# Kernel optimization log

Measured on AMD Instinct MI355X. Metric: run time of the kernel, lower is better.

## Reference

```python
import jax, jax.numpy as jnp
import numpy as np

PROCESSING_SPEED = 8.0  # init kwarg: softmax temperature
EPS = 1e-8              # torch F.cosine_similarity eps
BATCH, SIZE, DIM = 1024, 65536, 512


def setup_inputs() -> dict:
    key = jax.random.key(0)
    k1, k2 = jax.random.split(key)
    x = jax.random.normal(k1, (BATCH, DIM), dtype=jnp.float32)
    memory_bank = jax.random.normal(k2, (SIZE, DIM), dtype=jnp.float32)
    return {"x": x, "memory_bank": memory_bank}


def reference(x, memory_bank):
    # Cosine similarity between every query and every memory row, computed as
    # normalized dot products (math-equivalent to F.cosine_similarity with
    # denominator clamp max(||a||*||b||, eps), avoiding the (B,S,D) broadcast).
    x_norm = jnp.linalg.norm(x, axis=1, keepdims=True)            # (B, 1)
    m_norm = jnp.linalg.norm(memory_bank, axis=1, keepdims=True)  # (S, 1)
    dots = jnp.einsum('bd,sd->bs', x, memory_bank)                # (B, S)
    sims = dots / jnp.maximum(x_norm * m_norm.T, EPS)             # (B, S)
    attention = jax.nn.softmax(sims * PROCESSING_SPEED, axis=1)   # (B, S)
    return attention @ memory_bank                                # (B, D)
```

## Files before the change

### kernel.cpp

```cpp
#include <hip/hip_runtime.h>
#include <hip/hip_bf16.h>
#include <stdint.h>

#define B_N 1024
#define S_N 65536
#define D_N 512
#define SCALE 8.0f
#define KSPLIT 16
#define KCHUNK (S_N / KSPLIT)

typedef __attribute__((ext_vector_type(8))) short bf16x8;
typedef __attribute__((ext_vector_type(4))) float f32x4;

#define OFF_MBF   ((size_t)0)
#define OFF_MT    (OFF_MBF + (size_t)S_N * D_N * 2)
#define OFF_XBF   (OFF_MT  + (size_t)D_N * S_N * 2)
#define OFF_P     (OFF_XBF + (size_t)B_N * D_N * 2)
#define OFF_XNSQ  (OFF_P   + (size_t)B_N * S_N * 2)
#define OFF_MNSQ  (OFF_XNSQ + (size_t)B_N * 4)
#define OFF_LSUM  (OFF_MNSQ + (size_t)S_N * 4)
#define OFF_OPART (OFF_LSUM + (size_t)B_N * 4)

__device__ __forceinline__ unsigned short f2bf(float f) {
  unsigned u = __builtin_bit_cast(unsigned, f);
  u += 0x7fffu + ((u >> 16) & 1u);
  return (unsigned short)(u >> 16);
}

__device__ __forceinline__ void stage16(const unsigned short* g, unsigned short* l) {
  __builtin_amdgcn_global_load_lds(
      (const __attribute__((address_space(1))) void*)g,
      (__attribute__((address_space(3))) void*)l, 16, 0, 0);
}

__global__ void k_prep_x(const float* __restrict__ X, unsigned short* __restrict__ Xbf,
                         float* __restrict__ xnsq) {
  const int row = blockIdx.x;
  const int t = threadIdx.x;
  float4 v = ((const float4*)(X + (size_t)row * D_N))[t];
  float ss = v.x*v.x + v.y*v.y + v.z*v.z + v.w*v.w;
  ushort4 o; o.x = f2bf(v.x); o.y = f2bf(v.y); o.z = f2bf(v.z); o.w = f2bf(v.w);
  ((ushort4*)(Xbf + (size_t)row * D_N))[t] = o;
  #pragma unroll
  for (int m = 1; m < 64; m <<= 1) ss += __shfl_xor(ss, m);
  __shared__ float partial[2];
  if ((t & 63) == 0) partial[t >> 6] = ss;
  __syncthreads();
  if (t == 0) xnsq[row] = partial[0] + partial[1];
}

__global__ void k_prep_m(const float* __restrict__ M, unsigned short* __restrict__ Mbf,
                         unsigned short* __restrict__ Mt, float* __restrict__ mnsq) {
  __shared__ float ts[64 * 65];
  const int t = threadIdx.x;
  const int s0 = blockIdx.x * 64;
  const int r = t >> 2, cq = t & 3;
  const int c = t >> 2, sq = t & 3;
  float ss = 0.f;
  for (int ct = 0; ct < 8; ++ct) {
    float f[16];
    const float4* src = (const float4*)(M + (size_t)(s0 + r) * D_N + ct * 64 + cq * 16);
    #pragma unroll
    for (int k = 0; k < 4; ++k) {
      float4 v = src[k];
      f[4*k+0] = v.x; f[4*k+1] = v.y; f[4*k+2] = v.z; f[4*k+3] = v.w;
    }
    union { unsigned short u[16]; uint4 v4[2]; } pk;
    #pragma unroll
    for (int j = 0; j < 16; ++j) {
      ss += f[j] * f[j];
      pk.u[j] = f2bf(f[j]);
      ts[r * 65 + cq * 16 + j] = f[j];
    }
    uint4* dst = (uint4*)(Mbf + (size_t)(s0 + r) * D_N + ct * 64 + cq * 16);
    dst[0] = pk.v4[0]; dst[1] = pk.v4[1];
    __syncthreads();
    union { unsigned short u[16]; uint4 v4[2]; } pt;
    #pragma unroll
    for (int j = 0; j < 16; ++j) pt.u[j] = f2bf(ts[(sq * 16 + j) * 65 + c]);
    uint4* dt = (uint4*)(Mt + (size_t)(ct * 64 + c) * S_N + s0 + sq * 16);
    dt[0] = pt.v4[0]; dt[1] = pt.v4[1];
    __syncthreads();
  }
  ss += __shfl_xor(ss, 1);
  ss += __shfl_xor(ss, 2);
  if (cq == 0) mnsq[s0 + r] = ss;
}

__global__ __launch_bounds__(256, 2) void k_qk(
    const unsigned short* __restrict__ Xbf, const unsigned short* __restrict__ Mbf,
    const float* __restrict__ xnsq, const float* __restrict__ mnsq,
    unsigned short* __restrict__ P, float* __restrict__ lsum) {
  __shared__ unsigned short As[128 * 64];
  __shared__ unsigned short Bs[128 * 64];
  const int t = threadIdx.x;
  const int w = t >> 6, lane = t & 63, quad = lane >> 4, l15 = lane & 15;
  const int wr = w >> 1, wc = w & 1;
  const int x7 = l15 & 7;
  const int bm = blockIdx.x, bn = blockIdx.y;

  f32x4 acc[4][4];
  #pragma unroll
  for (int i = 0; i < 4; ++i)
    #pragma unroll
    for (int j = 0; j < 4; ++j) acc[i][j] = (f32x4){0.f, 0.f, 0.f, 0.f};

  const int srow = t >> 3;
  const int schunk = (t & 7) ^ (srow & 7);
  const unsigned short* gA = Xbf + (size_t)(bm * 128 + srow) * D_N + schunk * 8;
  const unsigned short* gB = Mbf + (size_t)(bn * 128 + srow) * D_N + schunk * 8;
  unsigned short* lA = As + w * 512;
  unsigned short* lB = Bs + w * 512;

  for (int k0 = 0; k0 < D_N; k0 += 64) {
    #pragma unroll
    for (int i = 0; i < 4; ++i) {
      stage16(gA + (size_t)(i * 32) * D_N + k0, lA + i * 2048);
      stage16(gB + (size_t)(i * 32) * D_N + k0, lB + i * 2048);
    }
    __syncthreads();
    #pragma unroll
    for (int kk = 0; kk < 64; kk += 32) {
      const int cq = (kk >> 3) + quad;
      bf16x8 af[4], bfr[4];
      #pragma unroll
      for (int i = 0; i < 4; ++i)
        af[i] = *(const bf16x8*)&As[(wr * 64 + i * 16 + l15) * 64 + (cq ^ x7) * 8];
      #pragma unroll
      for (int j = 0; j < 4; ++j)
        bfr[j] = *(const bf16x8*)&Bs[(wc * 64 + j * 16 + l15) * 64 + (cq ^ x7) * 8];
      #pragma unroll
      for (int i = 0; i < 4; ++i)
        #pragma unroll
        for (int j = 0; j < 4; ++j)
          acc[i][j] = __builtin_amdgcn_mfma_f32_16x16x32_bf16(af[i], bfr[j], acc[i][j], 0, 0, 0);
    }
    __syncthreads();
  }

  float mn_[4];
  #pragma unroll
  for (int j = 0; j < 4; ++j) mn_[j] = mnsq[bn * 128 + wc * 64 + j * 16 + l15];
  #pragma unroll
  for (int i = 0; i < 4; ++i) {
    float rowsum[4];
    #pragma unroll
    for (int r = 0; r < 4; ++r) {
      const int b = bm * 128 + wr * 64 + i * 16 + quad * 4 + r;
      const float xq = xnsq[b];
      float rs = 0.f;
      #pragma unroll
      for (int j = 0; j < 4; ++j) {
        float d2 = fmaxf(xq * mn_[j], 1e-16f);
        float p = __expf(SCALE * acc[i][j][r] * rsqrtf(d2));
        rs += p;
        const int s = bn * 128 + wc * 64 + j * 16 + l15;
        P[(size_t)b * S_N + s] = f2bf(p);
      }
      rowsum[r] = rs;
    }
    #pragma unroll
    for (int r = 0; r < 4; ++r) {
      float rs = rowsum[r];
      rs += __shfl_xor(rs, 1);
      rs += __shfl_xor(rs, 2);
      rs += __shfl_xor(rs, 4);
      rs += __shfl_xor(rs, 8);
      if (l15 == 0) {
        const int b = bm * 128 + wr * 64 + i * 16 + quad * 4 + r;
        unsafeAtomicAdd(&lsum[b], rs);
      }
    }
  }
}

__global__ __launch_bounds__(256, 2) void k_pv(
    const unsigned short* __restrict__ P, const unsigned short* __restrict__ Mt,
    float* __restrict__ Opart) {
  __shared__ unsigned short As[128 * 64];
  __shared__ unsigned short Bs[128 * 64];
  const int t = threadIdx.x;
  const int w = t >> 6, lane = t & 63, quad = lane >> 4, l15 = lane & 15;
  const int wr = w >> 1, wc = w & 1;
  const int x7 = l15 & 7;
  const int bn = blockIdx.x, bm = blockIdx.y, ks = blockIdx.z;

  f32x4 acc[4][4];
  #pragma unroll
  for (int i = 0; i < 4; ++i)
    #pragma unroll
    for (int j = 0; j < 4; ++j) acc[i][j] = (f32x4){0.f, 0.f, 0.f, 0.f};

  const int srow = t >> 3;
  const int schunk = (t & 7) ^ (srow & 7);
  const unsigned short* gA = P  + (size_t)(bm * 128 + srow) * S_N + (size_t)ks * KCHUNK + schunk * 8;
  const unsigned short* gB = Mt + (size_t)(bn * 128 + srow) * S_N + (size_t)ks * KCHUNK + schunk * 8;
  unsigned short* lA = As + w * 512;
  unsigned short* lB = Bs + w * 512;

  for (int k0 = 0; k0 < KCHUNK; k0 += 64) {
    #pragma unroll
    for (int i = 0; i < 4; ++i) {
      stage16(gA + (size_t)(i * 32) * S_N + k0, lA + i * 2048);
      stage16(gB + (size_t)(i * 32) * S_N + k0, lB + i * 2048);
    }
    __syncthreads();
    #pragma unroll
    for (int kk = 0; kk < 64; kk += 32) {
      const int cq = (kk >> 3) + quad;
      bf16x8 af[4], bfr[4];
      #pragma unroll
      for (int i = 0; i < 4; ++i)
        af[i] = *(const bf16x8*)&As[(wr * 64 + i * 16 + l15) * 64 + (cq ^ x7) * 8];
      #pragma unroll
      for (int j = 0; j < 4; ++j)
        bfr[j] = *(const bf16x8*)&Bs[(wc * 64 + j * 16 + l15) * 64 + (cq ^ x7) * 8];
      #pragma unroll
      for (int i = 0; i < 4; ++i)
        #pragma unroll
        for (int j = 0; j < 4; ++j)
          acc[i][j] = __builtin_amdgcn_mfma_f32_16x16x32_bf16(af[i], bfr[j], acc[i][j], 0, 0, 0);
    }
    __syncthreads();
  }

  float* Od = Opart + (size_t)ks * (B_N * D_N);
  #pragma unroll
  for (int i = 0; i < 4; ++i)
    #pragma unroll
    for (int r = 0; r < 4; ++r) {
      const int b = bm * 128 + wr * 64 + i * 16 + quad * 4 + r;
      #pragma unroll
      for (int j = 0; j < 4; ++j) {
        const int d = bn * 128 + wc * 64 + j * 16 + l15;
        Od[(size_t)b * D_N + d] = acc[i][j][r];
      }
    }
}

__global__ void k_combine(const float* __restrict__ Opart, const float* __restrict__ lsum,
                          float* __restrict__ out) {
  const int idx = blockIdx.x * 256 + threadIdx.x;
  const int b = idx >> 7;
  float4 s = {0.f, 0.f, 0.f, 0.f};
  #pragma unroll
  for (int ks = 0; ks < KSPLIT; ++ks) {
    float4 v = ((const float4*)Opart)[(size_t)ks * (B_N * D_N / 4) + idx];
    s.x += v.x; s.y += v.y; s.z += v.z; s.w += v.w;
  }
  const float inv = 1.0f / lsum[b];
  s.x *= inv; s.y *= inv; s.z *= inv; s.w *= inv;
  ((float4*)out)[idx] = s;
}

extern "C" void kernel_launch(void* const* d_in, const int* in_sizes, int n_in,
                              void* d_out, int out_size, void* d_ws, size_t ws_size,
                              hipStream_t stream) {
  const float* X = (const float*)d_in[0];
  const float* M = (const float*)d_in[1];
  char* ws = (char*)d_ws;
  unsigned short* Mbf  = (unsigned short*)(ws + OFF_MBF);
  unsigned short* Mt   = (unsigned short*)(ws + OFF_MT);
  unsigned short* Xbf  = (unsigned short*)(ws + OFF_XBF);
  unsigned short* P    = (unsigned short*)(ws + OFF_P);
  float* xnsq = (float*)(ws + OFF_XNSQ);
  float* mnsq = (float*)(ws + OFF_MNSQ);
  float* lsum = (float*)(ws + OFF_LSUM);
  float* Opart = (float*)(ws + OFF_OPART);

  hipMemsetAsync(lsum, 0, B_N * sizeof(float), stream);
  k_prep_x<<<dim3(B_N), 128, 0, stream>>>(X, Xbf, xnsq);
  k_prep_m<<<dim3(S_N / 64), 256, 0, stream>>>(M, Mbf, Mt, mnsq);
  k_qk<<<dim3(8, S_N / 128), 256, 0, stream>>>(Xbf, Mbf, xnsq, mnsq, P, lsum);
  k_pv<<<dim3(D_N / 128, B_N / 128, KSPLIT), 256, 0, stream>>>(P, Mt, Opart);
  k_combine<<<dim3(B_N * D_N / 4 / 256), 256, 0, stream>>>(Opart, lsum, (float*)d_out);
}
```

Baseline: 488.9 us.

## Fuse QK softmax and PV into one flash-style kernel keeping P in LDS

The separate QK kernel, which wrote the full bf16 probability matrix to global memory, and the PV kernel that read it back are replaced by a single fused kernel. That kernel computes a 128x128 score tile, exponentiates it into LDS, and immediately multiplies it by the transposed memory bank, accumulating output over a chunk of S. The softmax scale and log2e are folded into precomputed reciprocal norms so the kernel can use exp2f, and the split over S becomes 32 chunks with an XCD-aware block mapping. This removes roughly 128MB each of P writes and reads, at the cost of only 256 blocks of 512 threads, heavy accumulator register pressure, and more partial outputs for the combine step.

```diff
diff --git a/kernel.cpp b/kernel.cpp
--- a/kernel.cpp
+++ b/kernel.cpp
@@ -5,9 +5,10 @@
 #define B_N 1024
 #define S_N 65536
 #define D_N 512
-#define SCALE 8.0f
-#define KSPLIT 16
-#define KCHUNK (S_N / KSPLIT)
+#define NS 32
+#define SC (S_N / NS)
+#define SB 128
+#define NSUB (SC / SB)
 
 typedef __attribute__((ext_vector_type(8))) short bf16x8;
 typedef __attribute__((ext_vector_type(4))) float f32x4;
@@ -15,10 +16,9 @@
 #define OFF_MBF   ((size_t)0)
 #define OFF_MT    (OFF_MBF + (size_t)S_N * D_N * 2)
 #define OFF_XBF   (OFF_MT  + (size_t)D_N * S_N * 2)
-#define OFF_P     (OFF_XBF + (size_t)B_N * D_N * 2)
-#define OFF_XNSQ  (OFF_P   + (size_t)B_N * S_N * 2)
-#define OFF_MNSQ  (OFF_XNSQ + (size_t)B_N * 4)
-#define OFF_LSUM  (OFF_MNSQ + (size_t)S_N * 4)
+#define OFF_RX    (OFF_XBF + (size_t)B_N * D_N * 2)
+#define OFF_RM    (OFF_RX  + (size_t)B_N * 4)
+#define OFF_LSUM  (OFF_RM  + (size_t)S_N * 4)
 #define OFF_OPART (OFF_LSUM + (size_t)B_N * 4)
 
 __device__ __forceinline__ unsigned short f2bf(float f) {
@@ -34,7 +34,7 @@
 }
 
 __global__ void k_prep_x(const float* __restrict__ X, unsigned short* __restrict__ Xbf,
-                         float* __restrict__ xnsq) {
+                         float* __restrict__ rx) {
   const int row = blockIdx.x;
   const int t = threadIdx.x;
   float4 v = ((const float4*)(X + (size_t)row * D_N))[t];
@@ -46,11 +46,11 @@
   __shared__ float partial[2];
   if ((t & 63) == 0) partial[t >> 6] = ss;
   __syncthreads();
-  if (t == 0) xnsq[row] = partial[0] + partial[1];
+  if (t == 0) rx[row] = 11.541560327111707f * rsqrtf(fmaxf(partial[0] + partial[1], 1e-24f));
 }
 
 __global__ void k_prep_m(const float* __restrict__ M, unsigned short* __restrict__ Mbf,
-                         unsigned short* __restrict__ Mt, float* __restrict__ mnsq) {
+                         unsigned short* __restrict__ Mt, float* __restrict__ rm) {
   __shared__ float ts[64 * 65];
   const int t = threadIdx.x;
   const int s0 = blockIdx.x * 64;
@@ -84,158 +84,169 @@
   }
   ss += __shfl_xor(ss, 1);
   ss += __shfl_xor(ss, 2);
-  if (cq == 0) mnsq[s0 + r] = ss;
-}
-
-__global__ __launch_bounds__(256, 2) void k_qk(
+  if (cq == 0) rm[s0 + r] = rsqrtf(fmaxf(ss, 1e-24f));
+}
+
+__global__ __launch_bounds__(512, 2) void k_fused(
     const unsigned short* __restrict__ Xbf, const unsigned short* __restrict__ Mbf,
-    const float* __restrict__ xnsq, const float* __restrict__ mnsq,
-    unsigned short* __restrict__ P, float* __restrict__ lsum) {
-  __shared__ unsigned short As[128 * 64];
-  __shared__ unsigned short Bs[128 * 64];
+    const unsigned short* __restrict__ Mt, const float* __restrict__ rx,
+    const float* __restrict__ rminv, float* __restrict__ lsum,
+    float* __restrict__ Opart) {
+  __shared__ unsigned short smem[16384];
+  __shared__ unsigned short Ps[16384];
+
   const int t = threadIdx.x;
   const int w = t >> 6, lane = t & 63, quad = lane >> 4, l15 = lane & 15;
-  const int wr = w >> 1, wc = w & 1;
+  const int qr = w >> 1, qc = w & 1;
   const int x7 = l15 & 7;
-  const int bm = blockIdx.x, bn = blockIdx.y;
-
-  f32x4 acc[4][4];
-  #pragma unroll
-  for (int i = 0; i < 4; ++i)
-    #pragma unroll
-    for (int j = 0; j < 4; ++j) acc[i][j] = (f32x4){0.f, 0.f, 0.f, 0.f};
-
-  const int srow = t >> 3;
-  const int schunk = (t & 7) ^ (srow & 7);
-  const unsigned short* gA = Xbf + (size_t)(bm * 128 + srow) * D_N + schunk * 8;
-  const unsigned short* gB = Mbf + (size_t)(bn * 128 + srow) * D_N + schunk * 8;
-  unsigned short* lA = As + w * 512;
-  unsigned short* lB = Bs + w * 512;
-
-  for (int k0 = 0; k0 < D_N; k0 += 64) {
-    #pragma unroll
-    for (int i = 0; i < 4; ++i) {
-      stage16(gA + (size_t)(i * 32) * D_N + k0, lA + i * 2048);
-      stage16(gB + (size_t)(i * 32) * D_N + k0, lB + i * 2048);
+
+  const int bid = blockIdx.x;
+  const int xcd = bid & 7, slot = bid >> 3;
+  const int bblk = slot & 7;
+  const int chunk = xcd * 4 + (slot >> 3);
+  const int b0 = bblk * 128;
+  const int s0 = chunk * SC;
+
+  unsigned short* As = smem;
+  unsigned short* Bs = smem + 8192;
+
+  f32x4 accO[4][2][4];
+  #pragma unroll
+  for (int dc = 0; dc < 4; ++dc)
+    #pragma unroll
+    for (int i = 0; i < 2; ++i)
+      #pragma unroll
+      for (int j = 0; j < 4; ++j) accO[dc][i][j] = (f32x4){0.f, 0.f, 0.f, 0.f};
+
+  float ls[4] = {0.f, 0.f, 0.f, 0.f};
+  float rxj[4];
+  #pragma unroll
+  for (int j = 0; j < 4; ++j) rxj[j] = rx[b0 + qc * 64 + j * 16 + l15];
+
+  const int srow8 = t >> 3;
+  const int sch8  = ((t & 7) ^ (srow8 & 7)) * 8;
+  const unsigned short* gX = Xbf + (size_t)(b0 + srow8) * D_N + sch8;
+  const int mrow = t >> 4;
+  const int mch  = ((t & 15) ^ (mrow & 7)) * 8;
+
+  for (int sub = 0; sub < NSUB; ++sub) {
+    const int sS = s0 + sub * SB;
+
+    f32x4 accP[2][4];
+    #pragma unroll
+    for (int i = 0; i < 2; ++i)
+      #pragma unroll
+      for (int j = 0; j < 4; ++j) accP[i][j] = (f32x4){0.f, 0.f, 0.f, 0.f};
+
+    const unsigned short* gM = Mbf + (size_t)(sS + srow8) * D_N + sch8;
+    for (int k0 = 0; k0 < D_N; k0 += 64) {
+      stage16(gM + k0,                      As + w * 512);
+      stage16(gM + (size_t)64 * D_N + k0,   As + 4096 + w * 512);
+      stage16(gX + k0,                      Bs + w * 512);
+      stage16(gX + (size_t)64 * D_N + k0,   Bs + 4096 + w * 512);
+      __syncthreads();
+      #pragma unroll
+      for (int kk = 0; kk < 64; kk += 32) {
+        const int cq = (kk >> 3) + quad;
+        bf16x8 a[2], b[4];
+        #pragma unroll
+        for (int i = 0; i < 2; ++i)
+          a[i] = *(const bf16x8*)&As[(qr * 32 + i * 16 + l15) * 64 + ((cq ^ x7) << 3)];
+        #pragma unroll
+        for (int j = 0; j < 4; ++j)
+          b[j] = *(const bf16x8*)&Bs[(qc * 64 + j * 16 + l15) * 64 + ((cq ^ x7) << 3)];
+        #pragma unroll
+        for (int i = 0; i < 2; ++i)
+          #pragma unroll
+          for (int j = 0; j < 4; ++j)
+            accP[i][j] = __builtin_amdgcn_mfma_f32_16x16x32_bf16(a[i], b[j], accP[i][j], 0, 0, 0);
+      }
+      __syncthreads();
+    }
+
+    const float4 rm0 = *(const float4*)&rminv[sS + qr * 32 + quad * 4];
+    const float4 rm1 = *(const float4*)&rminv[sS + qr * 32 + 16 + quad * 4];
+    #pragma unroll
+    for (int i = 0; i < 2; ++i) {
+      const float4 rm = i ? rm1 : rm0;
+      const int sl  = qr * 32 + i * 16 + quad * 4;
+      const int c16 = sl >> 3;
+      const int o8  = (sl >> 2) & 1;
+      #pragma unroll
+      for (int j = 0; j < 4; ++j) {
+        const float p0 = exp2f(accP[i][j][0] * rxj[j] * rm.x);
+        const float p1 = exp2f(accP[i][j][1] * rxj[j] * rm.y);
+        const float p2 = exp2f(accP[i][j][2] * rxj[j] * rm.z);
+        const float p3 = exp2f(accP[i][j][3] * rxj[j] * rm.w);
+        ls[j] += (p0 + p1) + (p2 + p3);
+        const int brow = qc * 64 + j * 16 + l15;
+        uint2 pk;
+        pk.x = (unsigned)f2bf(p0) | ((unsigned)f2bf(p1) << 16);
+        pk.y = (unsigned)f2bf(p2) | ((unsigned)f2bf(p3) << 16);
+        *(uint2*)&Ps[brow * 128 + (((c16 ^ (brow & 7)) << 3) | (o8 << 2))] = pk;
+      }
     }
     __syncthreads();
-    #pragma unroll
-    for (int kk = 0; kk < 64; kk += 32) {
-      const int cq = (kk >> 3) + quad;
-      bf16x8 af[4], bfr[4];
-      #pragma unroll
-      for (int i = 0; i < 4; ++i)
-        af[i] = *(const bf16x8*)&As[(wr * 64 + i * 16 + l15) * 64 + (cq ^ x7) * 8];
-      #pragma unroll
-      for (int j = 0; j < 4; ++j)
-        bfr[j] = *(const bf16x8*)&Bs[(wc * 64 + j * 16 + l15) * 64 + (cq ^ x7) * 8];
-      #pragma unroll
-      for (int i = 0; i < 4; ++i)
+
+    #pragma unroll
+    for (int dc = 0; dc < 4; ++dc) {
+      const unsigned short* gT = Mt + (size_t)(dc * 128 + mrow) * S_N + sS + mch;
+      stage16(gT,                      smem + w * 512);
+      stage16(gT + (size_t)32 * S_N,   smem + 4096 + w * 512);
+      stage16(gT + (size_t)64 * S_N,   smem + 8192 + w * 512);
+      stage16(gT + (size_t)96 * S_N,   smem + 12288 + w * 512);
+      __syncthreads();
+      #pragma unroll
+      for (int kk = 0; kk < 128; kk += 32) {
+        const int cq = (kk >> 3) + quad;
+        bf16x8 pa[2], mb[4];
+        #pragma unroll
+        for (int i = 0; i < 2; ++i)
+          pa[i] = *(const bf16x8*)&Ps[(qr * 32 + i * 16 + l15) * 128 + ((cq ^ x7) << 3)];
         #pragma unroll
         for (int j = 0; j < 4; ++j)
-          acc[i][j] = __builtin_amdgcn_mfma_f32_16x16x32_bf16(af[i], bfr[j], acc[i][j], 0, 0, 0);
-    }
-    __syncthreads();
-  }
-
-  float mn_[4];
-  #pragma unroll
-  for (int j = 0; j < 4; ++j) mn_[j] = mnsq[bn * 128 + wc * 64 + j * 16 + l15];
-  #pragma unroll
-  for (int i = 0; i < 4; ++i) {
-    float rowsum[4];
-    #pragma unroll
-    for (int r = 0; r < 4; ++r) {
-      const int b = bm * 128 + wr * 64 + i * 16 + quad * 4 + r;
-      const float xq = xnsq[b];
-      float rs = 0.f;
-      #pragma unroll
-      for (int j = 0; j < 4; ++j) {
-        float d2 = fmaxf(xq * mn_[j], 1e-16f);
-        float p = __expf(SCALE * acc[i][j][r] * rsqrtf(d2));
-        rs += p;
-        const int s = bn * 128 + wc * 64 + j * 16 + l15;
-        P[(size_t)b * S_N + s] = f2bf(p);
-      }
-      rowsum[r] = rs;
-    }
-    #pragma unroll
-    for (int r = 0; r < 4; ++r) {
-      float rs = rowsum[r];
-      rs += __shfl_xor(rs, 1);
-      rs += __shfl_xor(rs, 2);
-      rs += __shfl_xor(rs, 4);
-      rs += __shfl_xor(rs, 8);
-      if (l15 == 0) {
-        const int b = bm * 128 + wr * 64 + i * 16 + quad * 4 + r;
-        unsafeAtomicAdd(&lsum[b], rs);
-      }
-    }
-  }
-}
-
-__global__ __launch_bounds__(256, 2) void k_pv(
-    const unsigned short* __restrict__ P, const unsigned short* __restrict__ Mt,
-    float* __restrict__ Opart) {
-  __shared__ unsigned short As[128 * 64];
-  __shared__ unsigned short Bs[128 * 64];
-  const int t = threadIdx.x;
-  const int w = t >> 6, lane = t & 63, quad = lane >> 4, l15 = lane & 15;
-  const int wr = w >> 1, wc = w & 1;
-  const int x7 = l15 & 7;
-  const int bn = blockIdx.x, bm = blockIdx.y, ks = blockIdx.z;
-
-  f32x4 acc[4][4];
-  #pragma unroll
-  for (int i = 0; i < 4; ++i)
-    #pragma unroll
-    for (int j = 0; j < 4; ++j) acc[i][j] = (f32x4){0.f, 0.f, 0.f, 0.f};
-
-  const int srow = t >> 3;
-  const int schunk = (t & 7) ^ (srow & 7);
-  const unsigned short* gA = P  + (size_t)(bm * 128 + srow) * S_N + (size_t)ks * KCHUNK + schunk * 8;
-  const unsigned short* gB = Mt + (size_t)(bn * 128 + srow) * S_N + (size_t)ks * KCHUNK + schunk * 8;
-  unsigned short* lA = As + w * 512;
-  unsigned short* lB = Bs + w * 512;
-
-  for (int k0 = 0; k0 < KCHUNK; k0 += 64) {
-    #pragma unroll
-    for (int i = 0; i < 4; ++i) {
-      stage16(gA + (size_t)(i * 32) * S_N + k0, lA + i * 2048);
-      stage16(gB + (size_t)(i * 32) * S_N + k0, lB + i * 2048);
-    }
-    __syncthreads();
-    #pragma unroll
-    for (int kk = 0; kk < 64; kk += 32) {
-      const int cq = (kk >> 3) + quad;
-      bf16x8 af[4], bfr[4];
-      #pragma unroll
-      for (int i = 0; i < 4; ++i)
-        af[i] = *(const bf16x8*)&As[(wr * 64 + i * 16 + l15) * 64 + (cq ^ x7) * 8];
-      #pragma unroll
-      for (int j = 0; j < 4; ++j)
-        bfr[j] = *(const bf16x8*)&Bs[(wc * 64 + j * 16 + l15) * 64 + (cq ^ x7) * 8];
-      #pragma unroll
-      for (int i = 0; i < 4; ++i)
-        #pragma unroll
-        for (int j = 0; j < 4; ++j)
-          acc[i][j] = __builtin_amdgcn_mfma_f32_16x16x32_bf16(af[i], bfr[j], acc[i][j], 0, 0, 0);
-    }
-    __syncthreads();
-  }
-
-  float* Od = Opart + (size_t)ks * (B_N * D_N);
-  #pragma unroll
-  for (int i = 0; i < 4; ++i)
-    #pragma unroll
-    for (int r = 0; r < 4; ++r) {
-      const int b = bm * 128 + wr * 64 + i * 16 + quad * 4 + r;
-      #pragma unroll
-      for (int j = 0; j < 4; ++j) {
-        const int d = bn * 128 + wc * 64 + j * 16 + l15;
-        Od[(size_t)b * D_N + d] = acc[i][j][r];
-      }
-    }
+          mb[j] = *(const bf16x8*)&smem[(qc * 64 + j * 16 + l15) * 128 + ((cq ^ x7) << 3)];
+        #pragma unroll
+        for (int i = 0; i < 2; ++i)
+          #pragma unroll
+          for (int j = 0; j < 4; ++j)
+            accO[dc][i][j] = __builtin_amdgcn_mfma_f32_16x16x32_bf16(pa[i], mb[j], accO[dc][i][j], 0, 0, 0);
+      }
+      __syncthreads();
+    }
+  }
+
+  float* Od = Opart + (size_t)chunk * ((size_t)B_N * D_N);
+  #pragma unroll
+  for (int dc = 0; dc < 4; ++dc)
+    #pragma unroll
+    for (int i = 0; i < 2; ++i)
+      #pragma unroll
+      for (int r = 0; r < 4; ++r) {
+        const int bb = b0 + qr * 32 + i * 16 + quad * 4 + r;
+        #pragma unroll
+        for (int j = 0; j < 4; ++j) {
+          const int d = dc * 128 + qc * 64 + j * 16 + l15;
+          Od[(size_t)bb * D_N + d] = accO[dc][i][j][r];
+        }
+      }
+
+  __syncthreads();
+  float* red = (float*)smem;
+  #pragma unroll
+  for (int j = 0; j < 4; ++j) {
+    float v = ls[j];
+    v += __shfl_xor(v, 16);
+    v += __shfl_xor(v, 32);
+    if (lane < 16) red[w * 64 + j * 16 + lane] = v;
+  }
+  __syncthreads();
+  if (t < 128) {
+    const int qc2 = t >> 6, idx = t & 63;
+    float s = red[(0 + qc2) * 64 + idx] + red[(2 + qc2) * 64 + idx] +
+              red[(4 + qc2) * 64 + idx] + red[(6 + qc2) * 64 + idx];
+    unsafeAtomicAdd(&lsum[b0 + t], s);
+  }
 }
 
 __global__ void k_combine(const float* __restrict__ Opart, const float* __restrict__ lsum,
@@ -244,7 +255,7 @@
   const int b = idx >> 7;
   float4 s = {0.f, 0.f, 0.f, 0.f};
   #pragma unroll
-  for (int ks = 0; ks < KSPLIT; ++ks) {
+  for (int ks = 0; ks < NS; ++ks) {
     float4 v = ((const float4*)Opart)[(size_t)ks * (B_N * D_N / 4) + idx];
     s.x += v.x; s.y += v.y; s.z += v.z; s.w += v.w;
   }
@@ -259,19 +270,17 @@
   const float* X = (const float*)d_in[0];
   const float* M = (const float*)d_in[1];
   char* ws = (char*)d_ws;
-  unsigned short* Mbf  = (unsigned short*)(ws + OFF_MBF);
-  unsigned short* Mt   = (unsigned short*)(ws + OFF_MT);
-  unsigned short* Xbf  = (unsigned short*)(ws + OFF_XBF);
-  unsigned short* P    = (unsigned short*)(ws + OFF_P);
-  float* xnsq = (float*)(ws + OFF_XNSQ);
-  float* mnsq = (float*)(ws + OFF_MNSQ);
+  unsigned short* Mbf = (unsigned short*)(ws + OFF_MBF);
+  unsigned short* Mt  = (unsigned short*)(ws + OFF_MT);
+  unsigned short* Xbf = (unsigned short*)(ws + OFF_XBF);
+  float* rxv  = (float*)(ws + OFF_RX);
+  float* rmv  = (float*)(ws + OFF_RM);
   float* lsum = (float*)(ws + OFF_LSUM);
   float* Opart = (float*)(ws + OFF_OPART);
 
   hipMemsetAsync(lsum, 0, B_N * sizeof(float), stream);
-  k_prep_x<<<dim3(B_N), 128, 0, stream>>>(X, Xbf, xnsq);
-  k_prep_m<<<dim3(S_N / 64), 256, 0, stream>>>(M, Mbf, Mt, mnsq);
-  k_qk<<<dim3(8, S_N / 128), 256, 0, stream>>>(Xbf, Mbf, xnsq, mnsq, P, lsum);
-  k_pv<<<dim3(D_N / 128, B_N / 128, KSPLIT), 256, 0, stream>>>(P, Mt, Opart);
+  k_prep_x<<<dim3(B_N), 128, 0, stream>>>(X, Xbf, rxv);
+  k_prep_m<<<dim3(S_N / 64), 256, 0, stream>>>(M, Mbf, Mt, rmv);
+  k_fused<<<dim3(8 * NS), 512, 0, stream>>>(Xbf, Mbf, Mt, rxv, rmv, lsum, Opart);
   k_combine<<<dim3(B_N * D_N / 4 / 256), 256, 0, stream>>>(Opart, lsum, (float*)d_out);
 }
```

Result: faster. 468.8 us (-4.1%).
